# Kernel optimization log

Measured on AMD Instinct MI355X. Metric: run time of the kernel, lower is better.

The kernel has to match this reference:

```python
import jax, jax.numpy as jnp
import numpy as np

B, IN, OUT, P, NS = 256, 1024, 512, 1000, 128

def setup_inputs() -> dict:
    key = jax.random.key(0)
    ks = jax.random.split(key, 6)
    return {
        "x": jax.random.normal(ks[0], (B, IN), jnp.float32),
        "noise": jax.random.normal(ks[1], (B, NS, P), jnp.float32),
        "fb_w": jax.random.normal(ks[2], (1, IN), jnp.float32) * (1.0 / np.sqrt(IN)),
        "fb_b": jnp.zeros((1,), jnp.float32),
        "decay_param": jnp.full((1,), 0.1, jnp.float32),
        "conv_w": jax.random.normal(ks[3], (P, P, 3), jnp.float32) * (1.0 / np.sqrt(3 * P)),
        "conv_b": jnp.zeros((P,), jnp.float32),
        "out_w": jax.random.normal(ks[4], (OUT, P), jnp.float32) * (1.0 / np.sqrt(P)),
        "out_b": jnp.zeros((OUT,), jnp.float32),
    }


def reference(x, noise, fb_w, fb_b, decay_param, conv_w, conv_b, out_w, out_b):
    # x: [B, IN]; noise: [B, NS, P] (Brownian increments for the SDE kernel)
    n_steps = noise.shape[1]
    dt = 1.0 / n_steps                       # T = 1.0
    sd = jnp.sqrt(jnp.asarray(dt, x.dtype))
    # per-sample feedback value: sigmoid(feedback_controller(x))
    feedback = jax.nn.sigmoid(x @ fb_w.T + fb_b)            # [B, 1]
    # decay value: sigmoid(decay_controller) * 0.5 (scalar)
    decay = jax.nn.sigmoid(decay_param[0]) * 0.5
    retain = 1.0 - decay * dt
    # Batched Euler-Maruyama Brownian SDE: X_{t+1} = (1 - decay*dt) X_t + feedback*sqrt(dt)*eps_t
    eps = jnp.transpose(noise, (1, 0, 2))                    # [NS, B, P]
    x0 = jnp.zeros((x.shape[0], noise.shape[2]), x.dtype)

    def step(X, e):
        Xn = X * retain + feedback * sd * e
        return Xn, Xn

    _, paths = jax.lax.scan(step, x0, eps)                   # [NS, B, P]
    paths_bct = jnp.transpose(paths, (1, 2, 0))              # [B, P, NS]
    # temporal_aggregator: Conv1d(P, P, kernel=3, padding=1) over time, then mean over time
    agg = jax.lax.conv_general_dilated(
        paths_bct, conv_w, window_strides=(1,), padding=[(1, 1)],
        dimension_numbers=("NCH", "OIH", "NCH"))
    agg = (agg + conv_b[None, :, None]).mean(axis=2)         # [B, P]
    # output_projection: P -> OUT
    return agg @ out_w.T + out_b
```

## Files before the change

kernel.cpp:

```cpp
#include <hip/hip_runtime.h>
#include <hip/hip_bf16.h>

#define B_N   256
#define IN_N  1024
#define OUT_N 512
#define P_N   1000
#define NS_N  128

#define K1P   3072
#define N1P   1024
#define K2P   1024
#define SK1   16
#define SK2   16

typedef __attribute__((ext_vector_type(8))) short short8v;
typedef __attribute__((ext_vector_type(4))) float f32x4;
typedef unsigned short ushort_t;
typedef __attribute__((ext_vector_type(4))) unsigned short ushort4v;

__device__ __forceinline__ float sigmoid_f(float z) { return 1.0f / (1.0f + __expf(-z)); }

__device__ __forceinline__ ushort_t f2bf(float x) {
    return __bfloat16_as_ushort(__float2bfloat16(x));
}
__device__ __forceinline__ float bf2f(ushort_t h) {
    union { unsigned u; float f; } v; v.u = ((unsigned)h) << 16;
    return v.f;
}
__device__ __forceinline__ unsigned pack2(float a, float b) {
    return (unsigned)f2bf(a) | ((unsigned)f2bf(b) << 16);
}

__global__ __launch_bounds__(512) void sde_fused_kernel(const float* __restrict__ x,
                                                        const float* __restrict__ fb_w,
                                                        const float* __restrict__ fb_b,
                                                        const float* __restrict__ noise,
                                                        const float* __restrict__ decay_param,
                                                        ushort_t* __restrict__ Thi) {
    const int b  = blockIdx.x;
    const int ch = blockIdx.y;
    const int t  = threadIdx.x;
    const int cg = t & 127;
    const int tq = t >> 7;

    float2 xv = ((const float2*)(x + (size_t)b * IN_N))[t];
    float2 wv = ((const float2*)fb_w)[t];
    float partial = xv.x * wv.x + xv.y * wv.y;
    #pragma unroll
    for (int o = 32; o >= 1; o >>= 1) partial += __shfl_down(partial, o, 64);
    __shared__ float wred[8];
    if ((t & 63) == 0) wred[t >> 6] = partial;
    __syncthreads();
    float fbs = wred[0] + wred[1] + wred[2] + wred[3] +
                wred[4] + wred[5] + wred[6] + wred[7];
    float fbv = sigmoid_f(fbs + fb_b[0]);

    float decay = sigmoid_f(decay_param[0]) * 0.5f;
    const float dt = 1.0f / NS_N;
    float retain = 1.0f - decay * dt;
    float inv_omr = 1.0f / (decay * dt);
    float r2 = retain * retain, r4 = r2 * r2, r8 = r4 * r4;
    float r16 = r8 * r8, r32 = r16 * r16;
    float r64 = r32 * r32, r96 = r64 * r32;

    const int c0 = ch * 512 + cg * 4;
    const bool act = (c0 < P_N);
    const float* base = noise + (size_t)b * NS_N * P_N + (act ? c0 : 0);

    float4 sE = {0, 0, 0, 0}, L = {0, 0, 0, 0};
    if (act) {
        const int s0 = tq * 32;
        float rp = 1.0f;
        #pragma unroll 8
        for (int ss = s0 + 31; ss >= s0; --ss) {
            float4 e = *(const float4*)(base + (size_t)ss * P_N);
            sE.x += e.x; sE.y += e.y; sE.z += e.z; sE.w += e.w;
            L.x += rp * e.x; L.y += rp * e.y; L.z += rp * e.z; L.w += rp * e.w;
            rp *= retain;
        }
    }

    __shared__ float4 xSE[3][128], xL[3][128], xF[128];
    if (tq < 3) { xSE[tq][cg] = sE; xL[tq][cg] = L; }
    if (tq == 0 && act) xF[cg] = *(const float4*)base;
    __syncthreads();

    if (tq == 3) {
        size_t tb = (size_t)b * K1P + 3 * (size_t)c0;
        uint2* tp = (uint2*)(Thi + tb);
        if (!act) {
            uint2 z2 = {0u, 0u};
            tp[0] = z2; tp[1] = z2; tp[2] = z2;
            return;
        }
        float4 se0 = xSE[0][cg], se1 = xSE[1][cg], se2 = xSE[2][cg];
        float4 l0 = xL[0][cg], l1 = xL[1][cg], l2 = xL[2][cg], ff = xF[cg];
        float Se[4] = {se0.x + se1.x + se2.x + sE.x, se0.y + se1.y + se2.y + sE.y,
                       se0.z + se1.z + se2.z + sE.z, se0.w + se1.w + se2.w + sE.w};
        float Lv[4] = {L.x + r32 * l2.x + r64 * l1.x + r96 * l0.x,
                       L.y + r32 * l2.y + r64 * l1.y + r96 * l0.y,
                       L.z + r32 * l2.z + r64 * l1.z + r96 * l0.z,
                       L.w + r32 * l2.w + r64 * l1.w + r96 * l0.w};
        float Fv[4] = {ff.x, ff.y, ff.z, ff.w};
        float sd = sqrtf(dt);
        float scale = fbv * sd * (1.0f / NS_N);
        float tv[12];
        #pragma unroll
        for (int j = 0; j < 4; ++j) {
            float Aj = (Se[j] - retain * Lv[j]) * inv_omr;
            tv[3 * j + 0] = scale * (Aj - Lv[j]);
            tv[3 * j + 1] = scale * Aj;
            tv[3 * j + 2] = scale * (Aj - Fv[j]);
        }
        uint2 o0 = {pack2(tv[0], tv[1]), pack2(tv[2], tv[3])};
        uint2 o1 = {pack2(tv[4], tv[5]), pack2(tv[6], tv[7])};
        uint2 o2 = {pack2(tv[8], tv[9]), pack2(tv[10], tv[11])};
        tp[0] = o0; tp[1] = o1; tp[2] = o2;
    }
}

__global__ __launch_bounds__(512) void gemm_bf16_bm256(const ushort_t* __restrict__ A,
                                                       const float* __restrict__ B,
                                                       ushort_t* __restrict__ Cpart,
                                                       int lda, int ldb,
                                                       int Nvalid, int Kvalid,
                                                       int Kper, int ldc) {
    __shared__ __align__(16) ushort_t As[256 * 64];
    __shared__ __align__(16) ushort_t Bs[128 * 64];

    const int tid  = threadIdx.x;
    const int lane = tid & 63;
    const int wave = tid >> 6;
    const int r15  = lane & 15;
    const int g4   = lane >> 4;
    const int wrow = wave >> 1;
    const int wcol = wave & 1;
    const int bid  = blockIdx.x;
    const int z    = bid & 15;
    const int n0   = (bid >> 4) * 128;
    const int kbeg = z * Kper;

    f32x4 acc[4][4] = {};

    for (int kt = 0; kt < Kper; kt += 64) {
        const int kk0 = kbeg + kt;
        #pragma unroll
        for (int c = 0; c < 4; ++c) {
            int ci = c * 512 + tid;
            int row = ci >> 3;
            int gs  = ci & 7;
            int g   = gs ^ (row & 7);
            const ushort_t* src = A + (size_t)row * lda + kk0 + g * 8;
            __builtin_amdgcn_global_load_lds(
                (const __attribute__((address_space(1))) void*)src,
                (__attribute__((address_space(3))) void*)&As[(size_t)(c * 512 + wave * 64) * 8],
                16, 0, 0);
        }
        #pragma unroll
        for (int c = 0; c < 2; ++c) {
            int chunk = tid + c * 512;
            int row = chunk >> 3, g = chunk & 7;
            int ldsoff = row * 64 + ((g ^ (row & 7)) << 3);
            int k = kk0 + g * 8;
            short8v bh = {0, 0, 0, 0, 0, 0, 0, 0};
            if ((n0 + row) < Nvalid && k < Kvalid) {
                const float* bp = B + (size_t)(n0 + row) * ldb + k;
                float4 b0 = *(const float4*)bp;
                float4 b1 = *(const float4*)(bp + 4);
                bh[0] = (short)f2bf(b0.x); bh[1] = (short)f2bf(b0.y);
                bh[2] = (short)f2bf(b0.z); bh[3] = (short)f2bf(b0.w);
                bh[4] = (short)f2bf(b1.x); bh[5] = (short)f2bf(b1.y);
                bh[6] = (short)f2bf(b1.z); bh[7] = (short)f2bf(b1.w);
            }
            *(short8v*)&Bs[ldsoff] = bh;
        }
        __syncthreads();

        #pragma unroll
        for (int ks = 0; ks < 2; ++ks) {
            const int g = ks * 4 + g4;
            short8v af[4], bfv[4];
            #pragma unroll
            for (int f = 0; f < 4; ++f) {
                int arow = wrow * 64 + f * 16 + r15;
                af[f] = *(const short8v*)&As[arow * 64 + ((g ^ (arow & 7)) << 3)];
            }
            #pragma unroll
            for (int f = 0; f < 4; ++f) {
                int brow = wcol * 64 + f * 16 + r15;
                bfv[f] = *(const short8v*)&Bs[brow * 64 + ((g ^ (brow & 7)) << 3)];
            }
            #pragma unroll
            for (int mf = 0; mf < 4; ++mf) {
                #pragma unroll
                for (int nf = 0; nf < 4; ++nf) {
                    acc[mf][nf] = __builtin_amdgcn_mfma_f32_16x16x32_bf16(af[mf], bfv[nf], acc[mf][nf], 0, 0, 0);
                }
            }
        }
        __syncthreads();
    }

    ushort_t* cp = Cpart + (size_t)z * B_N * ldc;
    #pragma unroll
    for (int mf = 0; mf < 4; ++mf) {
        #pragma unroll
        for (int nf = 0; nf < 4; ++nf) {
            #pragma unroll
            for (int r = 0; r < 4; ++r) {
                int m = wrow * 64 + mf * 16 + g4 * 4 + r;
                int n = n0 + wcol * 64 + nf * 16 + r15;
                cp[(size_t)m * ldc + n] = f2bf(acc[mf][nf][r]);
            }
        }
    }
}

__global__ __launch_bounds__(256) void reduce_agg_kernel(const ushort_t* __restrict__ Cpart1,
                                                         const float* __restrict__ conv_b,
                                                         ushort_t* __restrict__ agg) {
    int idx4 = (blockIdx.x * 256 + threadIdx.x) * 4;
    int n = idx4 & (N1P - 1);
    float s0 = 0.f, s1 = 0.f, s2 = 0.f, s3 = 0.f;
    if (n < P_N) {
        float4 cb = *(const float4*)(conv_b + n);
        s0 = cb.x; s1 = cb.y; s2 = cb.z; s3 = cb.w;
        #pragma unroll
        for (int z = 0; z < SK1; ++z) {
            ushort4v p = *(const ushort4v*)(Cpart1 + (size_t)z * (B_N * N1P) + idx4);
            s0 += bf2f(p[0]); s1 += bf2f(p[1]); s2 += bf2f(p[2]); s3 += bf2f(p[3]);
        }
    }
    ushort4v o = {f2bf(s0), f2bf(s1), f2bf(s2), f2bf(s3)};
    *(ushort4v*)(agg + idx4) = o;
}

__global__ __launch_bounds__(256) void reduce_out_kernel(const ushort_t* __restrict__ Cpart2,
                                                         const float* __restrict__ out_b,
                                                         float* __restrict__ out) {
    int idx4 = (blockIdx.x * 256 + threadIdx.x) * 4;
    int n = idx4 & (OUT_N - 1);
    float4 ob = *(const float4*)(out_b + n);
    float s0 = ob.x, s1 = ob.y, s2 = ob.z, s3 = ob.w;
    #pragma unroll
    for (int z = 0; z < SK2; ++z) {
        ushort4v p = *(const ushort4v*)(Cpart2 + (size_t)z * (B_N * OUT_N) + idx4);
        s0 += bf2f(p[0]); s1 += bf2f(p[1]); s2 += bf2f(p[2]); s3 += bf2f(p[3]);
    }
    float4 o = {s0, s1, s2, s3};
    *(float4*)(out + idx4) = o;
}

extern "C" void kernel_launch(void* const* d_in, const int* in_sizes, int n_in,
                              void* d_out, int out_size, void* d_ws, size_t ws_size,
                              hipStream_t stream) {
    const float* x           = (const float*)d_in[0];
    const float* noise       = (const float*)d_in[1];
    const float* fb_w        = (const float*)d_in[2];
    const float* fb_b        = (const float*)d_in[3];
    const float* decay_param = (const float*)d_in[4];
    const float* conv_w      = (const float*)d_in[5];
    const float* conv_b      = (const float*)d_in[6];
    const float* out_w       = (const float*)d_in[7];
    const float* out_b       = (const float*)d_in[8];
    float* out = (float*)d_out;

    char* ws = (char*)d_ws;
    size_t off = 0;
    ushort_t* Thi    = (ushort_t*)(ws + off); off += (size_t)B_N * K1P * 2;
    ushort_t* agg    = (ushort_t*)(ws + off); off += (size_t)B_N * K2P * 2;
    ushort_t* Cpart1 = (ushort_t*)(ws + off); off += (size_t)SK1 * B_N * N1P * 2;
    ushort_t* Cpart2 = (ushort_t*)(ws + off); off += (size_t)SK2 * B_N * OUT_N * 2;

    {
        dim3 grid(B_N, 2);
        sde_fused_kernel<<<grid, 512, 0, stream>>>(x, fb_w, fb_b, noise, decay_param, Thi);
    }

    gemm_bf16_bm256<<<dim3(N1P / 128 * SK1), 512, 0, stream>>>(Thi, conv_w, Cpart1,
                                                               K1P, 3 * P_N, P_N, 3 * P_N,
                                                               K1P / SK1, N1P);

    reduce_agg_kernel<<<(B_N * N1P) / 1024, 256, 0, stream>>>(Cpart1, conv_b, agg);

    gemm_bf16_bm256<<<dim3(OUT_N / 128 * SK2), 512, 0, stream>>>(agg, out_w, Cpart2,
                                                                 K2P, P_N, OUT_N, P_N,
                                                                 K2P / SK2, OUT_N);

    reduce_out_kernel<<<(B_N * OUT_N) / 1024, 256, 0, stream>>>(Cpart2, out_b, out);
}
```

Before: 45.57 us.

## Fuse split-K partial reduction of first GEMM into second GEMM's A-tile load

Result: no change. 46.01 us (+1.0%).

```diff
diff --git a/kernel.cpp b/kernel.cpp
--- a/kernel.cpp
+++ b/kernel.cpp
@@ -216,23 +216,103 @@
     }
 }
 
-__global__ __launch_bounds__(256) void reduce_agg_kernel(const ushort_t* __restrict__ Cpart1,
-                                                         const float* __restrict__ conv_b,
-                                                         ushort_t* __restrict__ agg) {
-    int idx4 = (blockIdx.x * 256 + threadIdx.x) * 4;
-    int n = idx4 & (N1P - 1);
-    float s0 = 0.f, s1 = 0.f, s2 = 0.f, s3 = 0.f;
-    if (n < P_N) {
-        float4 cb = *(const float4*)(conv_b + n);
-        s0 = cb.x; s1 = cb.y; s2 = cb.z; s3 = cb.w;
-        #pragma unroll
-        for (int z = 0; z < SK1; ++z) {
-            ushort4v p = *(const ushort4v*)(Cpart1 + (size_t)z * (B_N * N1P) + idx4);
-            s0 += bf2f(p[0]); s1 += bf2f(p[1]); s2 += bf2f(p[2]); s3 += bf2f(p[3]);
-        }
-    }
-    ushort4v o = {f2bf(s0), f2bf(s1), f2bf(s2), f2bf(s3)};
-    *(ushort4v*)(agg + idx4) = o;
+__global__ __launch_bounds__(512) void gemm2_fused_agg(const ushort_t* __restrict__ Cpart1,
+                                                       const float* __restrict__ conv_b,
+                                                       const float* __restrict__ out_w,
+                                                       ushort_t* __restrict__ Cpart2) {
+    __shared__ __align__(16) ushort_t As[64 * 64];
+    __shared__ __align__(16) ushort_t Bs[512 * 64];
+
+    const int tid  = threadIdx.x;
+    const int lane = tid & 63;
+    const int wave = tid >> 6;
+    const int r15  = lane & 15;
+    const int g4   = lane >> 4;
+    const int bid  = blockIdx.x;
+    const int z    = bid & 15;
+    const int m0   = (bid >> 4) * 64;
+    const int k0   = z * 64;
+
+    {
+        int row = tid >> 3, g = tid & 7;
+        int ldsoff = row * 64 + ((g ^ (row & 7)) << 3);
+        int k = k0 + g * 8;
+        short8v ah = {0, 0, 0, 0, 0, 0, 0, 0};
+        if (k < P_N) {
+            float s[8];
+            float4 c0v = *(const float4*)(conv_b + k);
+            float4 c1v = *(const float4*)(conv_b + k + 4);
+            s[0] = c0v.x; s[1] = c0v.y; s[2] = c0v.z; s[3] = c0v.w;
+            s[4] = c1v.x; s[5] = c1v.y; s[6] = c1v.z; s[7] = c1v.w;
+            size_t o = (size_t)(m0 + row) * N1P + k;
+            #pragma unroll
+            for (int zz = 0; zz < SK1; ++zz) {
+                short8v p = *(const short8v*)(Cpart1 + (size_t)zz * (B_N * N1P) + o);
+                #pragma unroll
+                for (int j = 0; j < 8; ++j) s[j] += bf2f((ushort_t)p[j]);
+            }
+            #pragma unroll
+            for (int j = 0; j < 8; ++j) ah[j] = (short)f2bf(s[j]);
+        }
+        *(short8v*)&As[ldsoff] = ah;
+    }
+    #pragma unroll
+    for (int c = 0; c < 8; ++c) {
+        int chunk = tid + c * 512;
+        int row = chunk >> 3, g = chunk & 7;
+        int ldsoff = row * 64 + ((g ^ (row & 7)) << 3);
+        int k = k0 + g * 8;
+        short8v bh = {0, 0, 0, 0, 0, 0, 0, 0};
+        if (k < P_N) {
+            const float* bp = out_w + (size_t)row * P_N + k;
+            float4 b0 = *(const float4*)bp;
+            float4 b1 = *(const float4*)(bp + 4);
+            bh[0] = (short)f2bf(b0.x); bh[1] = (short)f2bf(b0.y);
+            bh[2] = (short)f2bf(b0.z); bh[3] = (short)f2bf(b0.w);
+            bh[4] = (short)f2bf(b1.x); bh[5] = (short)f2bf(b1.y);
+            bh[6] = (short)f2bf(b1.z); bh[7] = (short)f2bf(b1.w);
+        }
+        *(short8v*)&Bs[ldsoff] = bh;
+    }
+    __syncthreads();
+
+    f32x4 acc[4][4] = {};
+    #pragma unroll
+    for (int ks = 0; ks < 2; ++ks) {
+        const int g = ks * 4 + g4;
+        short8v af[4], bfv[4];
+        #pragma unroll
+        for (int f = 0; f < 4; ++f) {
+            int arow = f * 16 + r15;
+            af[f] = *(const short8v*)&As[arow * 64 + ((g ^ (arow & 7)) << 3)];
+        }
+        #pragma unroll
+        for (int f = 0; f < 4; ++f) {
+            int brow = wave * 64 + f * 16 + r15;
+            bfv[f] = *(const short8v*)&Bs[brow * 64 + ((g ^ (brow & 7)) << 3)];
+        }
+        #pragma unroll
+        for (int mf = 0; mf < 4; ++mf) {
+            #pragma unroll
+            for (int nf = 0; nf < 4; ++nf) {
+                acc[mf][nf] = __builtin_amdgcn_mfma_f32_16x16x32_bf16(af[mf], bfv[nf], acc[mf][nf], 0, 0, 0);
+            }
+        }
+    }
+
+    ushort_t* cp = Cpart2 + (size_t)z * (B_N * OUT_N);
+    #pragma unroll
+    for (int mf = 0; mf < 4; ++mf) {
+        #pragma unroll
+        for (int nf = 0; nf < 4; ++nf) {
+            #pragma unroll
+            for (int r = 0; r < 4; ++r) {
+                int m = m0 + mf * 16 + g4 * 4 + r;
+                int n = wave * 64 + nf * 16 + r15;
+                cp[(size_t)m * OUT_N + n] = f2bf(acc[mf][nf][r]);
+            }
+        }
+    }
 }
 
 __global__ __launch_bounds__(256) void reduce_out_kernel(const ushort_t* __restrict__ Cpart2,
@@ -268,7 +348,6 @@
     char* ws = (char*)d_ws;
     size_t off = 0;
     ushort_t* Thi    = (ushort_t*)(ws + off); off += (size_t)B_N * K1P * 2;
-    ushort_t* agg    = (ushort_t*)(ws + off); off += (size_t)B_N * K2P * 2;
     ushort_t* Cpart1 = (ushort_t*)(ws + off); off += (size_t)SK1 * B_N * N1P * 2;
     ushort_t* Cpart2 = (ushort_t*)(ws + off); off += (size_t)SK2 * B_N * OUT_N * 2;
 
@@ -281,11 +360,7 @@
                                                                K1P, 3 * P_N, P_N, 3 * P_N,
                                                                K1P / SK1, N1P);
 
-    reduce_agg_kernel<<<(B_N * N1P) / 1024, 256, 0, stream>>>(Cpart1, conv_b, agg);
-
-    gemm_bf16_bm256<<<dim3(OUT_N / 128 * SK2), 512, 0, stream>>>(agg, out_w, Cpart2,
-                                                                 K2P, P_N, OUT_N, P_N,
-                                                                 K2P / SK2, OUT_N);
+    gemm2_fused_agg<<<dim3(4 * SK2), 512, 0, stream>>>(Cpart1, conv_b, out_w, Cpart2);
 
     reduce_out_kernel<<<(B_N * OUT_N) / 1024, 256, 0, stream>>>(Cpart2, out_b, out);
 }
```
